# Optimization experiments

Measured on AMD Instinct MI355X. Metric: run time of the kernel, lower is better.

## Reference

```python
import jax, jax.numpy as jnp
import numpy as np

N, L, C, H = 8, 2048, 512, 512
C_HALF = max(C // 2, 1)


def setup_inputs() -> dict:
    key = jax.random.key(0)
    ks = jax.random.split(key, 11)
    s = 0.02
    return {
        "x": jax.random.normal(ks[0], (N, L, C), dtype=jnp.float32),
        "theta_w": jax.random.normal(ks[1], (C, H), dtype=jnp.float32) * s,
        "theta_b": jax.random.normal(ks[2], (H,), dtype=jnp.float32) * s,
        "phi_w": jax.random.normal(ks[3], (C, H), dtype=jnp.float32) * s,
        "phi_b": jax.random.normal(ks[4], (H,), dtype=jnp.float32) * s,
        "psi_w": jax.random.normal(ks[5], (C, H), dtype=jnp.float32) * s,
        "psi_b": jax.random.normal(ks[6], (H,), dtype=jnp.float32) * s,
        "r1_w": jax.random.normal(ks[7], (H, C_HALF), dtype=jnp.float32) * s,
        "r1_b": jax.random.normal(ks[8], (C_HALF,), dtype=jnp.float32) * s,
        "r2_w": jax.random.normal(ks[9], (C_HALF, C), dtype=jnp.float32) * s,
        "r2_b": jax.random.normal(ks[10], (C,), dtype=jnp.float32) * s,
    }


def reference(x, theta_w, theta_b, phi_w, phi_b, psi_w, psi_b, r1_w, r1_b, r2_w, r2_b):
    # projections: [n, L, h]
    x_t = x @ theta_w + theta_b
    x_ph = x @ phi_w + phi_b
    x_psi = x @ psi_w + psi_b
    # unscaled attention: phi @ theta^T -> [n, L, L], softmax over last dim
    attn = jax.nn.softmax(jnp.einsum("nlh,nmh->nlm", x_ph, x_t), axis=2)
    x_add = jnp.einsum("nlm,nmh->nlh", attn, x_psi)
    # recover MLP with LeakyReLU(0.2) then Tanh, residual add
    h1 = jax.nn.leaky_relu(x_add @ r1_w + r1_b, negative_slope=0.2)
    h2 = jnp.tanh(h1 @ r2_w + r2_b)
    return x + h2
```

## Files before the change

kernel.cpp:

```cpp
#include <hip/hip_runtime.h>
#include <hip/hip_bf16.h>

typedef float f32x4 __attribute__((ext_vector_type(4)));
typedef int   v8i   __attribute__((ext_vector_type(8)));
typedef __attribute__((address_space(3))) unsigned int       lds_uint;
typedef __attribute__((address_space(1))) const unsigned int glb_uint;

__device__ __forceinline__ float tanh_fast(float x) {
    float e = __expf(-2.0f * fabsf(x));
    float r = (1.0f - e) / (1.0f + e);
    return copysignf(r, x);
}
__device__ __forceinline__ unsigned char f2fp8(float v) {
    return (unsigned char)(__builtin_amdgcn_cvt_pk_fp8_f32(v, 0.0f, 0, false) & 0xff);
}
__device__ __forceinline__ unsigned short f2h(float v) {
    _Float16 h = (_Float16)v;
    unsigned short u;
    __builtin_memcpy(&u, &h, 2);
    return u;
}
__device__ __forceinline__ float h2f(unsigned short u) {
    _Float16 h;
    __builtin_memcpy(&h, &u, 2);
    return (float)h;
}

__global__ __launch_bounds__(256) void prep(
    const float* __restrict__ x,
    const float* __restrict__ theta_w, const float* __restrict__ phi_w,
    const float* __restrict__ psi_w,   const float* __restrict__ r1_w,
    const float* __restrict__ r2_w,
    const float* __restrict__ theta_b, const float* __restrict__ phi_b,
    const float* __restrict__ psi_b,
    unsigned char* __restrict__ xb8, unsigned char* __restrict__ wCat8T,
    unsigned char* __restrict__ r1T8, unsigned char* __restrict__ r2T8,
    float* __restrict__ bCat) {
    const int b = blockIdx.x, t = threadIdx.x;
    if (b < 8192) {
        long i = ((long)b * 256 + t) * 4;
        float4 f = *(const float4*)(x + i);
        int w = __builtin_amdgcn_cvt_pk_fp8_f32(f.x, f.y, 0, false);
        w = __builtin_amdgcn_cvt_pk_fp8_f32(f.z, f.w, w, true);
        *(unsigned int*)(xb8 + i) = (unsigned int)w;
    } else if (b < 11264) {
        const int sel = (b - 8192) >> 10;
        const int idx = ((b - 8192) & 1023) * 256 + t;
        const float* w = sel == 0 ? theta_w : (sel == 1 ? phi_w : psi_w);
        const int r = idx >> 9, c = idx & 511;
        wCat8T[(long)(sel * 512 + c) * 512 + r] = f2fp8(w[idx] * 16.0f);
    } else if (b < 11776) {
        const int idx = (b - 11264) * 256 + t;
        const int r = idx >> 8, c = idx & 255;
        r1T8[(long)c * 512 + r] = f2fp8(r1_w[idx] * 16.0f);
    } else if (b < 12288) {
        const int idx = (b - 11776) * 256 + t;
        const int r = idx >> 9, c = idx & 511;
        r2T8[(long)c * 256 + r] = f2fp8(r2_w[idx] * 16.0f);
    } else {
        const int i = (b - 12288) * 256 + t;
        if (i < 1536)
            bCat[i] = i < 512 ? theta_b[i] : (i < 1024 ? phi_b[i - 512] : psi_b[i - 1024]);
    }
}

__global__ __launch_bounds__(256) void softmax_fp8(unsigned short* __restrict__ S) {
    const size_t row = (size_t)blockIdx.y * 2048 + blockIdx.x;
    unsigned short* p = S + row * 2048;
    const int t = threadIdx.x;
    uint4 raw = *(uint4*)(p + t * 8);
    unsigned int w[4] = {raw.x, raw.y, raw.z, raw.w};
    float v[8];
#pragma unroll
    for (int i = 0; i < 4; ++i) {
        v[2 * i]     = h2f((unsigned short)(w[i] & 0xffffu));
        v[2 * i + 1] = h2f((unsigned short)(w[i] >> 16));
    }
    float mx = v[0];
#pragma unroll
    for (int i = 1; i < 8; ++i) mx = fmaxf(mx, v[i]);
#pragma unroll
    for (int off = 32; off > 0; off >>= 1) mx = fmaxf(mx, __shfl_xor(mx, off));
    __shared__ float red[8];
    const int wave = t >> 6, lane = t & 63;
    if (lane == 0) red[wave] = mx;
    __syncthreads();
    mx = fmaxf(fmaxf(red[0], red[1]), fmaxf(red[2], red[3]));
    float s = 0.0f;
#pragma unroll
    for (int i = 0; i < 8; ++i) { v[i] = __expf(v[i] - mx); s += v[i]; }
#pragma unroll
    for (int off = 32; off > 0; off >>= 1) s += __shfl_xor(s, off);
    if (lane == 0) red[4 + wave] = s;
    __syncthreads();
    s = red[4] + red[5] + red[6] + red[7];
    const float inv = 1.0f / s;
    int o0 = __builtin_amdgcn_cvt_pk_fp8_f32(v[0] * inv, v[1] * inv, 0, false);
    o0 = __builtin_amdgcn_cvt_pk_fp8_f32(v[2] * inv, v[3] * inv, o0, true);
    int o1 = __builtin_amdgcn_cvt_pk_fp8_f32(v[4] * inv, v[5] * inv, 0, false);
    o1 = __builtin_amdgcn_cvt_pk_fp8_f32(v[6] * inv, v[7] * inv, o1, true);
    uint2 ov; ov.x = (unsigned int)o0; ov.y = (unsigned int)o1;
    *(uint2*)((unsigned char*)p + t * 8) = ov;
}

template <int MODE>
__global__ __launch_bounds__(256) void gemm_fp8(
    const unsigned char* __restrict__ A,
    const unsigned char* __restrict__ Bt,
    const float* __restrict__ bias,
    const float* __restrict__ resid,
    unsigned short* __restrict__ outH,
    unsigned char* __restrict__ out8,
    unsigned char* __restrict__ out8b,
    unsigned char* __restrict__ outV,
    float* __restrict__ outF,
    int K, int ldaB, int ldbB, int ldc, long sA, long sB, long sC) {
    __shared__ unsigned char As[2][128 * 128];
    __shared__ unsigned char Bs[2][128 * 128];

    const int tid  = threadIdx.x;
    const int lane = tid & 63, wave = tid >> 6;
    const int m16  = lane & 15, quad = lane >> 4;
    const int wm   = (wave >> 1) << 6, wn = (wave & 1) << 6;
    const int m0   = blockIdx.x << 7, n0 = blockIdx.y << 7;

    const int srow = lane >> 3;
    const int uswz = (lane & 7) ^ srow;

    const unsigned char* Abase = A  + (long)blockIdx.z * sA + (long)m0 * ldaB;
    const unsigned char* Bbase = Bt + (long)blockIdx.z * sB + (long)n0 * ldbB;
    const int stR = (wave << 5) + srow;
    const long gA0 = (long)stR * ldaB + (uswz << 4);
    const long gB0 = (long)stR * ldbB + (uswz << 4);

    const int s8  = m16 & 7;
    const int P   = quad ^ (s8 >> 1);
    const int cLo = (P << 1) + (s8 & 1);
    const int offLo = cLo << 4;
    const int offHi = (cLo ^ 1) << 4;

    f32x4 acc[4][4] = {};

    union F8 { v8i v; int4 q[2]; };

    auto STAGE = [&](int buf, int kk) {
#pragma unroll
        for (int i = 0; i < 4; ++i) {
            const unsigned char* gp = Abase + gA0 + (long)(i << 3) * ldaB + kk;
            unsigned char* lp = &As[buf][((wave << 5) + (i << 3)) << 7];
            __builtin_amdgcn_global_load_lds((glb_uint*)gp, (lds_uint*)lp, 16, 0, 0);
        }
#pragma unroll
        for (int i = 0; i < 4; ++i) {
            const unsigned char* gp = Bbase + gB0 + (long)(i << 3) * ldbB + kk;
            unsigned char* lp = &Bs[buf][((wave << 5) + (i << 3)) << 7];
            __builtin_amdgcn_global_load_lds((glb_uint*)gp, (lds_uint*)lp, 16, 0, 0);
        }
    };

    STAGE(0, 0);
    int cur = 0;
    for (int k0 = 0; k0 < K; k0 += 128) {
        if (k0 + 128 < K) {
            STAGE(cur ^ 1, k0 + 128);
            asm volatile("s_waitcnt vmcnt(8)" ::: "memory");
        } else {
            asm volatile("s_waitcnt vmcnt(0)" ::: "memory");
        }
        asm volatile("s_barrier" ::: "memory");

        const unsigned char* Ab = As[cur];
        const unsigned char* Bb = Bs[cur];
        F8 af[4], bg[4];
#pragma unroll
        for (int f = 0; f < 4; ++f) {
            const int m = wm + (f << 4) + m16;
            const int n = wn + (f << 4) + m16;
            af[f].q[0] = *(const int4*)&Ab[(m << 7) + offLo];
            af[f].q[1] = *(const int4*)&Ab[(m << 7) + offHi];
            bg[f].q[0] = *(const int4*)&Bb[(n << 7) + offLo];
            bg[f].q[1] = *(const int4*)&Bb[(n << 7) + offHi];
        }
#pragma unroll
        for (int fi = 0; fi < 4; ++fi)
#pragma unroll
            for (int fj = 0; fj < 4; ++fj)
                acc[fi][fj] = __builtin_amdgcn_mfma_scale_f32_16x16x128_f8f6f4(
                    af[fi].v, bg[fj].v, acc[fi][fj],
                    0, 0,
                    0, 127,
                    0, 127);

        asm volatile("s_waitcnt lgkmcnt(0)" ::: "memory");
        asm volatile("s_barrier" ::: "memory");
        cur ^= 1;
    }

    const long zC = (long)blockIdx.z * sC;

    if (MODE == 0) {
        const int sel = n0 >> 9;
        if (sel < 2) {
            unsigned char* dst = sel == 0 ? out8 : out8b;
#pragma unroll
            for (int fj = 0; fj < 4; ++fj) {
                const int col = n0 + wn + (fj << 4) + m16;
                const int cb  = col & 511;
                const float bv = bias[col];
#pragma unroll
                for (int fi = 0; fi < 4; ++fi)
#pragma unroll
                    for (int r = 0; r < 4; ++r) {
                        const int row = m0 + wm + (fi << 4) + (quad << 2) + r;
                        dst[(long)row * 512 + cb] = f2fp8(acc[fi][fj][r] * 0.0625f + bv);
                    }
            }
        } else {
            const int z = m0 >> 11, l0 = (m0 & 2047) + wm + (quad << 2);
#pragma unroll
            for (int fj = 0; fj < 4; ++fj) {
                const int col = n0 + wn + (fj << 4) + m16;
                const int h   = col & 511;
                const float bv = bias[col];
#pragma unroll
                for (int fi = 0; fi < 4; ++fi) {
                    int w = __builtin_amdgcn_cvt_pk_fp8_f32(
                        acc[fi][fj][0] * 0.0625f + bv, acc[fi][fj][1] * 0.0625f + bv, 0, false);
                    w = __builtin_amdgcn_cvt_pk_fp8_f32(
                        acc[fi][fj][2] * 0.0625f + bv, acc[fi][fj][3] * 0.0625f + bv, w, true);
                    *(unsigned int*)(outV + ((long)z * 512 + h) * 2048 + l0 + (fi << 4)) =
                        (unsigned int)w;
                }
            }
        }
    } else {
#pragma unroll
        for (int fj = 0; fj < 4; ++fj) {
            const int col = n0 + wn + (fj << 4) + m16;
            float bv = 0.0f;
            if (MODE >= 3) bv = bias[col];
#pragma unroll
            for (int fi = 0; fi < 4; ++fi)
#pragma unroll
                for (int r = 0; r < 4; ++r) {
                    const int row = m0 + wm + (fi << 4) + (quad << 2) + r;
                    float v = acc[fi][fj][r];
                    if (MODE == 1) {
                        outH[zC + (long)row * ldc + col] = f2h(v);
                    } else if (MODE == 2) {
                        out8[zC + (long)row * 512 + col] = f2fp8(v);
                    } else if (MODE == 3) {
                        v = v * 0.0625f + bv;
                        v = v > 0.0f ? v : 0.2f * v;
                        out8[(long)row * 256 + col] = f2fp8(v);
                    } else {
                        v = v * 0.0625f + bv;
                        const long idx = (long)row * ldc + col;
                        outF[idx] = tanh_fast(v) + resid[idx];
                    }
                }
        }
    }
}

extern "C" void kernel_launch(void* const* d_in, const int* in_sizes, int n_in,
                              void* d_out, int out_size, void* d_ws, size_t ws_size,
                              hipStream_t stream) {
    const float* x       = (const float*)d_in[0];
    const float* theta_w = (const float*)d_in[1];
    const float* theta_b = (const float*)d_in[2];
    const float* phi_w   = (const float*)d_in[3];
    const float* phi_b   = (const float*)d_in[4];
    const float* psi_w   = (const float*)d_in[5];
    const float* psi_b   = (const float*)d_in[6];
    const float* r1_w    = (const float*)d_in[7];
    const float* r1_b    = (const float*)d_in[8];
    const float* r2_w    = (const float*)d_in[9];
    const float* r2_b    = (const float*)d_in[10];
    float* out = (float*)d_out;

    constexpr int  N = 8, L = 2048, C = 512, H = 512, CH = 256;
    constexpr long NL = (long)N * L;

    char* p = (char*)d_ws;
    auto alloc = [&](size_t bytes) { void* q = (void*)p; p += bytes; return q; };
    unsigned char*  xb8    = (unsigned char*)alloc(NL * C);
    unsigned char*  TH8    = (unsigned char*)alloc(NL * H);
    unsigned char*  PH8    = (unsigned char*)alloc(NL * H);
    unsigned char*  VT8    = (unsigned char*)alloc((long)N * H * L);
    unsigned char*  xadd8  = (unsigned char*)alloc(NL * H);
    unsigned char*  h18    = (unsigned char*)alloc(NL * CH);
    unsigned char*  wCat8T = (unsigned char*)alloc((long)1536 * 512);
    unsigned char*  r1T8   = (unsigned char*)alloc((long)H * CH);
    unsigned char*  r2T8   = (unsigned char*)alloc((long)CH * C);
    float*          bCat   = (float*)alloc(1536 * 4 + 256);
    unsigned short* S      = (unsigned short*)alloc((long)N * L * L * 2);

    prep<<<12294, 256, 0, stream>>>(x, theta_w, phi_w, psi_w, r1_w, r2_w,
                                    theta_b, phi_b, psi_b, xb8, wCat8T, r1T8, r2T8, bCat);

    gemm_fp8<0><<<dim3(NL / 128, 1536 / 128, 1), 256, 0, stream>>>(
        xb8, wCat8T, bCat, nullptr, nullptr, TH8, PH8, VT8, nullptr,
        C, C, C, 0, 0, 0, 0);

    gemm_fp8<1><<<dim3(L / 128, L / 128, N), 256, 0, stream>>>(
        PH8, TH8, nullptr, nullptr, S, nullptr, nullptr, nullptr, nullptr,
        H, H, H, L, (long)L * H, (long)L * H, (long)L * L);

    softmax_fp8<<<dim3(L, N), 256, 0, stream>>>(S);

    gemm_fp8<2><<<dim3(L / 128, H / 128, N), 256, 0, stream>>>(
        (const unsigned char*)S, VT8, nullptr, nullptr, nullptr, xadd8, nullptr, nullptr, nullptr,
        L, 2 * L, L, H, (long)L * 2 * L, (long)H * L, (long)L * H);

    gemm_fp8<3><<<dim3(NL / 128, CH / 128, 1), 256, 0, stream>>>(
        xadd8, r1T8, r1_b, nullptr, nullptr, h18, nullptr, nullptr, nullptr,
        H, H, H, CH, 0, 0, 0);

    gemm_fp8<4><<<dim3(NL / 128, C / 128, 1), 256, 0, stream>>>(
        h18, r2T8, r2_b, x, nullptr, nullptr, nullptr, nullptr, out,
        CH, CH, CH, C, 0, 0, 0);
}
```

Baseline: 223.6 us.

## Add 256x256-tile 512-thread GEMM for projection and score stages

Adds a new fp8 GEMM kernel that uses 256x256 output tiles with 8 waves, each computing a 128x64 sub-tile. It is used for the fused QKV projection and for the phi·theta^T score GEMM, and it loads A fragments one at a time inside the loop to limit register pressure. Larger tiles raise data reuse per byte staged in LDS. The cost is 128KB of double-buffered LDS per block, which limits occupancy to one block per CU despite the launch bounds, and the grid has fewer blocks. The smaller GEMMs keep the 128x128 kernel, whose epilogue is trimmed to their modes.

```diff
diff --git a/kernel.cpp b/kernel.cpp
--- a/kernel.cpp
+++ b/kernel.cpp
@@ -109,10 +109,7 @@
     const unsigned char* __restrict__ Bt,
     const float* __restrict__ bias,
     const float* __restrict__ resid,
-    unsigned short* __restrict__ outH,
     unsigned char* __restrict__ out8,
-    unsigned char* __restrict__ out8b,
-    unsigned char* __restrict__ outV,
     float* __restrict__ outF,
     int K, int ldaB, int ldbB, int ldc, long sA, long sB, long sC) {
     __shared__ unsigned char As[2][128 * 128];
@@ -140,7 +137,6 @@
     const int offHi = (cLo ^ 1) << 4;
 
     f32x4 acc[4][4] = {};
-
     union F8 { v8i v; int4 q[2]; };
 
     auto STAGE = [&](int buf, int kk) {
@@ -187,9 +183,126 @@
             for (int fj = 0; fj < 4; ++fj)
                 acc[fi][fj] = __builtin_amdgcn_mfma_scale_f32_16x16x128_f8f6f4(
                     af[fi].v, bg[fj].v, acc[fi][fj],
-                    0, 0,
-                    0, 127,
-                    0, 127);
+                    0, 0, 0, 127, 0, 127);
+
+        asm volatile("s_waitcnt lgkmcnt(0)" ::: "memory");
+        asm volatile("s_barrier" ::: "memory");
+        cur ^= 1;
+    }
+
+    const long zC = (long)blockIdx.z * sC;
+
+#pragma unroll
+    for (int fj = 0; fj < 4; ++fj) {
+        const int col = n0 + wn + (fj << 4) + m16;
+        float bv = 0.0f;
+        if (MODE >= 3) bv = bias[col];
+#pragma unroll
+        for (int fi = 0; fi < 4; ++fi)
+#pragma unroll
+            for (int r = 0; r < 4; ++r) {
+                const int row = m0 + wm + (fi << 4) + (quad << 2) + r;
+                float v = acc[fi][fj][r];
+                if (MODE == 2) {
+                    out8[zC + (long)row * 512 + col] = f2fp8(v);
+                } else if (MODE == 3) {
+                    v = v * 0.0625f + bv;
+                    v = v > 0.0f ? v : 0.2f * v;
+                    out8[(long)row * 256 + col] = f2fp8(v);
+                } else {
+                    v = v * 0.0625f + bv;
+                    const long idx = (long)row * ldc + col;
+                    outF[idx] = tanh_fast(v) + resid[idx];
+                }
+            }
+    }
+}
+
+template <int MODE>
+__global__ __launch_bounds__(512, 2) void gemm_fp8_big(
+    const unsigned char* __restrict__ A,
+    const unsigned char* __restrict__ Bt,
+    const float* __restrict__ bias,
+    unsigned short* __restrict__ outH,
+    unsigned char* __restrict__ out8,
+    unsigned char* __restrict__ out8b,
+    unsigned char* __restrict__ outV,
+    int K, int ldaB, int ldbB, int ldc, long sA, long sB, long sC) {
+    __shared__ unsigned char As[2][256 * 128];
+    __shared__ unsigned char Bs[2][256 * 128];
+
+    const int tid  = threadIdx.x;
+    const int lane = tid & 63, wave = tid >> 6;
+    const int m16  = lane & 15, quad = lane >> 4;
+    const int wm   = (wave >> 2) << 7;
+    const int wn   = (wave & 3) << 6;
+    const int m0   = blockIdx.x << 8, n0 = blockIdx.y << 8;
+
+    const int srow = lane >> 3;
+    const int uswz = (lane & 7) ^ srow;
+
+    const unsigned char* Abase = A  + (long)blockIdx.z * sA + (long)m0 * ldaB;
+    const unsigned char* Bbase = Bt + (long)blockIdx.z * sB + (long)n0 * ldbB;
+    const int stR = (wave << 5) + srow;
+    const long gA0 = (long)stR * ldaB + (uswz << 4);
+    const long gB0 = (long)stR * ldbB + (uswz << 4);
+
+    const int s8  = m16 & 7;
+    const int P   = quad ^ (s8 >> 1);
+    const int cLo = (P << 1) + (s8 & 1);
+    const int offLo = cLo << 4;
+    const int offHi = (cLo ^ 1) << 4;
+
+    f32x4 acc[8][4] = {};
+    union F8 { v8i v; int4 q[2]; };
+
+    auto STAGE = [&](int buf, int kk) {
+#pragma unroll
+        for (int i = 0; i < 4; ++i) {
+            const unsigned char* gp = Abase + gA0 + (long)(i << 3) * ldaB + kk;
+            unsigned char* lp = &As[buf][((wave << 5) + (i << 3)) << 7];
+            __builtin_amdgcn_global_load_lds((glb_uint*)gp, (lds_uint*)lp, 16, 0, 0);
+        }
+#pragma unroll
+        for (int i = 0; i < 4; ++i) {
+            const unsigned char* gp = Bbase + gB0 + (long)(i << 3) * ldbB + kk;
+            unsigned char* lp = &Bs[buf][((wave << 5) + (i << 3)) << 7];
+            __builtin_amdgcn_global_load_lds((glb_uint*)gp, (lds_uint*)lp, 16, 0, 0);
+        }
+    };
+
+    STAGE(0, 0);
+    int cur = 0;
+    for (int k0 = 0; k0 < K; k0 += 128) {
+        if (k0 + 128 < K) {
+            STAGE(cur ^ 1, k0 + 128);
+            asm volatile("s_waitcnt vmcnt(8)" ::: "memory");
+        } else {
+            asm volatile("s_waitcnt vmcnt(0)" ::: "memory");
+        }
+        asm volatile("s_barrier" ::: "memory");
+
+        const unsigned char* Ab = As[cur];
+        const unsigned char* Bb = Bs[cur];
+        F8 bg[4];
+#pragma unroll
+        for (int fj = 0; fj < 4; ++fj) {
+            const int n = wn + (fj << 4) + m16;
+            bg[fj].q[0] = *(const int4*)&Bb[(n << 7) + offLo];
+            bg[fj].q[1] = *(const int4*)&Bb[(n << 7) + offHi];
+        }
+#pragma unroll
+        for (int fi = 0; fi < 8; ++fi) {
+            F8 af;
+            const int m = wm + (fi << 4) + m16;
+            af.q[0] = *(const int4*)&Ab[(m << 7) + offLo];
+            af.q[1] = *(const int4*)&Ab[(m << 7) + offHi];
+#pragma unroll
+            for (int fj = 0; fj < 4; ++fj)
+                acc[fi][fj] = __builtin_amdgcn_mfma_scale_f32_16x16x128_f8f6f4(
+                    af.v, bg[fj].v, acc[fi][fj],
+                    0, 0, 0, 127, 0, 127);
+        }
 
         asm volatile("s_waitcnt lgkmcnt(0)" ::: "memory");
         asm volatile("s_barrier" ::: "memory");
@@ -208,7 +321,7 @@
                 const int cb  = col & 511;
                 const float bv = bias[col];
 #pragma unroll
-                for (int fi = 0; fi < 4; ++fi)
+                for (int fi = 0; fi < 8; ++fi)
 #pragma unroll
                     for (int r = 0; r < 4; ++r) {
                         const int row = m0 + wm + (fi << 4) + (quad << 2) + r;
@@ -223,7 +336,7 @@
                 const int h   = col & 511;
                 const float bv = bias[col];
 #pragma unroll
-                for (int fi = 0; fi < 4; ++fi) {
+                for (int fi = 0; fi < 8; ++fi) {
                     int w = __builtin_amdgcn_cvt_pk_fp8_f32(
                         acc[fi][fj][0] * 0.0625f + bv, acc[fi][fj][1] * 0.0625f + bv, 0, false);
                     w = __builtin_amdgcn_cvt_pk_fp8_f32(
@@ -237,27 +350,12 @@
 #pragma unroll
         for (int fj = 0; fj < 4; ++fj) {
             const int col = n0 + wn + (fj << 4) + m16;
-            float bv = 0.0f;
-            if (MODE >= 3) bv = bias[col];
-#pragma unroll
-            for (int fi = 0; fi < 4; ++fi)
+#pragma unroll
+            for (int fi = 0; fi < 8; ++fi)
 #pragma unroll
                 for (int r = 0; r < 4; ++r) {
                     const int row = m0 + wm + (fi << 4) + (quad << 2) + r;
-                    float v = acc[fi][fj][r];
-                    if (MODE == 1) {
-                        outH[zC + (long)row * ldc + col] = f2h(v);
-                    } else if (MODE == 2) {
-                        out8[zC + (long)row * 512 + col] = f2fp8(v);
-                    } else if (MODE == 3) {
-                        v = v * 0.0625f + bv;
-                        v = v > 0.0f ? v : 0.2f * v;
-                        out8[(long)row * 256 + col] = f2fp8(v);
-                    } else {
-                        v = v * 0.0625f + bv;
-                        const long idx = (long)row * ldc + col;
-                        outF[idx] = tanh_fast(v) + resid[idx];
-                    }
+                    outH[zC + (long)row * ldc + col] = f2h(acc[fi][fj][r]);
                 }
         }
     }
@@ -299,25 +397,25 @@
     prep<<<12294, 256, 0, stream>>>(x, theta_w, phi_w, psi_w, r1_w, r2_w,
                                     theta_b, phi_b, psi_b, xb8, wCat8T, r1T8, r2T8, bCat);
 
-    gemm_fp8<0><<<dim3(NL / 128, 1536 / 128, 1), 256, 0, stream>>>(
-        xb8, wCat8T, bCat, nullptr, nullptr, TH8, PH8, VT8, nullptr,
+    gemm_fp8_big<0><<<dim3(NL / 256, 1536 / 256, 1), 512, 0, stream>>>(
+        xb8, wCat8T, bCat, nullptr, TH8, PH8, VT8,
         C, C, C, 0, 0, 0, 0);
 
-    gemm_fp8<1><<<dim3(L / 128, L / 128, N), 256, 0, stream>>>(
-        PH8, TH8, nullptr, nullptr, S, nullptr, nullptr, nullptr, nullptr,
+    gemm_fp8_big<1><<<dim3(L / 256, L / 256, N), 512, 0, stream>>>(
+        PH8, TH8, nullptr, S, nullptr, nullptr, nullptr,
         H, H, H, L, (long)L * H, (long)L * H, (long)L * L);
 
     softmax_fp8<<<dim3(L, N), 256, 0, stream>>>(S);
 
     gemm_fp8<2><<<dim3(L / 128, H / 128, N), 256, 0, stream>>>(
-        (const unsigned char*)S, VT8, nullptr, nullptr, nullptr, xadd8, nullptr, nullptr, nullptr,
+        (const unsigned char*)S, VT8, nullptr, nullptr, xadd8, nullptr,
         L, 2 * L, L, H, (long)L * 2 * L, (long)H * L, (long)L * H);
 
     gemm_fp8<3><<<dim3(NL / 128, CH / 128, 1), 256, 0, stream>>>(
-        xadd8, r1T8, r1_b, nullptr, nullptr, h18, nullptr, nullptr, nullptr,
+        xadd8, r1T8, r1_b, nullptr, h18, nullptr,
         H, H, H, CH, 0, 0, 0);
 
     gemm_fp8<4><<<dim3(NL / 128, C / 128, 1), 256, 0, stream>>>(
-        h18, r2T8, r2_b, x, nullptr, nullptr, nullptr, nullptr, out,
+        h18, r2T8, r2_b, x, nullptr, out,
         CH, CH, CH, C, 0, 0, 0);
 }
```

Result: no change. 227.9 us (+1.9%).

## Fuse attention score, softmax and PV GEMMs into a flash-attention kernel

Applied to the files above, without the earlier changes.

Replaces the separate QK^T GEMM, the fp16 score write, the softmax pass and the PV GEMM with one flash-style kernel that keeps scores on chip and uses an online softmax with running max and sum. This removes the round trips of the 8x2048x2048 score matrix through global memory and two kernel launches. In exchange the new kernel uses 512-thread blocks with large LDS buffers, only 256 blocks, and many barriers per chunk, so occupancy and sync overhead could limit it. P is rescaled by 256 before fp8 conversion to keep precision.

```diff
diff --git a/kernel.cpp b/kernel.cpp
--- a/kernel.cpp
+++ b/kernel.cpp
@@ -13,17 +13,6 @@
 }
 __device__ __forceinline__ unsigned char f2fp8(float v) {
     return (unsigned char)(__builtin_amdgcn_cvt_pk_fp8_f32(v, 0.0f, 0, false) & 0xff);
-}
-__device__ __forceinline__ unsigned short f2h(float v) {
-    _Float16 h = (_Float16)v;
-    unsigned short u;
-    __builtin_memcpy(&u, &h, 2);
-    return u;
-}
-__device__ __forceinline__ float h2f(unsigned short u) {
-    _Float16 h;
-    __builtin_memcpy(&h, &u, 2);
-    return (float)h;
 }
 
 __global__ __launch_bounds__(256) void prep(
@@ -64,52 +53,12 @@
     }
 }
 
-__global__ __launch_bounds__(256) void softmax_fp8(unsigned short* __restrict__ S) {
-    const size_t row = (size_t)blockIdx.y * 2048 + blockIdx.x;
-    unsigned short* p = S + row * 2048;
-    const int t = threadIdx.x;
-    uint4 raw = *(uint4*)(p + t * 8);
-    unsigned int w[4] = {raw.x, raw.y, raw.z, raw.w};
-    float v[8];
-#pragma unroll
-    for (int i = 0; i < 4; ++i) {
-        v[2 * i]     = h2f((unsigned short)(w[i] & 0xffffu));
-        v[2 * i + 1] = h2f((unsigned short)(w[i] >> 16));
-    }
-    float mx = v[0];
-#pragma unroll
-    for (int i = 1; i < 8; ++i) mx = fmaxf(mx, v[i]);
-#pragma unroll
-    for (int off = 32; off > 0; off >>= 1) mx = fmaxf(mx, __shfl_xor(mx, off));
-    __shared__ float red[8];
-    const int wave = t >> 6, lane = t & 63;
-    if (lane == 0) red[wave] = mx;
-    __syncthreads();
-    mx = fmaxf(fmaxf(red[0], red[1]), fmaxf(red[2], red[3]));
-    float s = 0.0f;
-#pragma unroll
-    for (int i = 0; i < 8; ++i) { v[i] = __expf(v[i] - mx); s += v[i]; }
-#pragma unroll
-    for (int off = 32; off > 0; off >>= 1) s += __shfl_xor(s, off);
-    if (lane == 0) red[4 + wave] = s;
-    __syncthreads();
-    s = red[4] + red[5] + red[6] + red[7];
-    const float inv = 1.0f / s;
-    int o0 = __builtin_amdgcn_cvt_pk_fp8_f32(v[0] * inv, v[1] * inv, 0, false);
-    o0 = __builtin_amdgcn_cvt_pk_fp8_f32(v[2] * inv, v[3] * inv, o0, true);
-    int o1 = __builtin_amdgcn_cvt_pk_fp8_f32(v[4] * inv, v[5] * inv, 0, false);
-    o1 = __builtin_amdgcn_cvt_pk_fp8_f32(v[6] * inv, v[7] * inv, o1, true);
-    uint2 ov; ov.x = (unsigned int)o0; ov.y = (unsigned int)o1;
-    *(uint2*)((unsigned char*)p + t * 8) = ov;
-}
-
 template <int MODE>
 __global__ __launch_bounds__(256) void gemm_fp8(
     const unsigned char* __restrict__ A,
     const unsigned char* __restrict__ Bt,
     const float* __restrict__ bias,
     const float* __restrict__ resid,
-    unsigned short* __restrict__ outH,
     unsigned char* __restrict__ out8,
     unsigned char* __restrict__ out8b,
     unsigned char* __restrict__ outV,
@@ -140,7 +89,6 @@
     const int offHi = (cLo ^ 1) << 4;
 
     f32x4 acc[4][4] = {};
-
     union F8 { v8i v; int4 q[2]; };
 
     auto STAGE = [&](int buf, int kk) {
@@ -187,16 +135,12 @@
             for (int fj = 0; fj < 4; ++fj)
                 acc[fi][fj] = __builtin_amdgcn_mfma_scale_f32_16x16x128_f8f6f4(
                     af[fi].v, bg[fj].v, acc[fi][fj],
-                    0, 0,
-                    0, 127,
-                    0, 127);
+                    0, 0, 0, 127, 0, 127);
 
         asm volatile("s_waitcnt lgkmcnt(0)" ::: "memory");
         asm volatile("s_barrier" ::: "memory");
         cur ^= 1;
     }
-
-    const long zC = (long)blockIdx.z * sC;
 
     if (MODE == 0) {
         const int sel = n0 >> 9;
@@ -237,30 +181,256 @@
 #pragma unroll
         for (int fj = 0; fj < 4; ++fj) {
             const int col = n0 + wn + (fj << 4) + m16;
-            float bv = 0.0f;
-            if (MODE >= 3) bv = bias[col];
+            const float bv = bias[col];
 #pragma unroll
             for (int fi = 0; fi < 4; ++fi)
 #pragma unroll
                 for (int r = 0; r < 4; ++r) {
                     const int row = m0 + wm + (fi << 4) + (quad << 2) + r;
-                    float v = acc[fi][fj][r];
-                    if (MODE == 1) {
-                        outH[zC + (long)row * ldc + col] = f2h(v);
-                    } else if (MODE == 2) {
-                        out8[zC + (long)row * 512 + col] = f2fp8(v);
-                    } else if (MODE == 3) {
-                        v = v * 0.0625f + bv;
+                    float v = acc[fi][fj][r] * 0.0625f + bv;
+                    if (MODE == 3) {
                         v = v > 0.0f ? v : 0.2f * v;
                         out8[(long)row * 256 + col] = f2fp8(v);
                     } else {
-                        v = v * 0.0625f + bv;
                         const long idx = (long)row * ldc + col;
                         outF[idx] = tanh_fast(v) + resid[idx];
                     }
                 }
         }
     }
+}
+
+__global__ __launch_bounds__(512) void flash(
+    const unsigned char* __restrict__ Qg8,
+    const unsigned char* __restrict__ Kg8,
+    const unsigned char* __restrict__ Vg8,
+    unsigned char* __restrict__ out8) {
+    __shared__ unsigned char Qs[64 * 512];
+    __shared__ unsigned char Ks[2][128 * 128];
+    __shared__ unsigned char Vs[512 * 128];
+    __shared__ unsigned char Ps[64 * 128];
+    __shared__ float smax[2][32][4];
+    __shared__ float ssum[2][32][4];
+
+    const int tid  = threadIdx.x;
+    const int lane = tid & 63, wave = tid >> 6;
+    const int m16  = lane & 15, quad = lane >> 4;
+    const int lg   = wave >> 2;
+    const int mw   = wave & 3;
+    const int z    = blockIdx.y;
+    const int l0   = blockIdx.x << 6;
+
+    const unsigned char* Qg = Qg8 + ((long)z * 2048 + l0) * 512;
+    const unsigned char* Kg = Kg8 + (long)z * 2048 * 512;
+    const unsigned char* Vg = Vg8 + (long)z * 512 * 2048;
+
+    const int s8  = m16 & 7;
+    const int cLo = ((quad ^ (s8 >> 1)) << 1) + (s8 & 1);
+    const int offLo = cLo << 4, offHi = (cLo ^ 1) << 4;
+
+    auto stageQ = [&]() {
+#pragma unroll
+        for (int i = 0; i < 4; ++i) {
+            const int slot = wave * 4 + i;
+            const int row  = slot * 2 + (lane >> 5);
+            const int w5   = lane & 31;
+            const int su   = (w5 & 24) | ((w5 & 7) ^ (row & 7));
+            const unsigned char* gp = Qg + (long)row * 512 + (su << 4);
+            __builtin_amdgcn_global_load_lds((glb_uint*)gp, (lds_uint*)&Qs[slot << 10], 16, 0, 0);
+        }
+    };
+    auto stageK = [&](int t) {
+        const int c = t >> 2, ks = t & 3;
+#pragma unroll
+        for (int i = 0; i < 2; ++i) {
+            const int slot = wave * 2 + i;
+            const int row  = (slot << 3) + (lane >> 3);
+            const int su   = (lane & 7) ^ (row & 7);
+            const unsigned char* gp = Kg + (long)(c * 128 + row) * 512 + ks * 128 + (su << 4);
+            __builtin_amdgcn_global_load_lds((glb_uint*)gp, (lds_uint*)&Ks[t & 1][slot << 10], 16, 0, 0);
+        }
+    };
+    auto stageV = [&](int c) {
+#pragma unroll
+        for (int i = 0; i < 8; ++i) {
+            const int slot = wave * 8 + i;
+            const int row  = (slot << 3) + (lane >> 3);
+            const int su   = (lane & 7) ^ (row & 7);
+            const unsigned char* gp = Vg + (long)row * 2048 + c * 128 + (su << 4);
+            __builtin_amdgcn_global_load_lds((glb_uint*)gp, (lds_uint*)&Vs[slot << 10], 16, 0, 0);
+        }
+    };
+
+    f32x4 U[2][8] = {};
+    float m_run[2][4], l_run[2][4];
+#pragma unroll
+    for (int a = 0; a < 2; ++a)
+#pragma unroll
+        for (int b = 0; b < 4; ++b) { m_run[a][b] = -3.0e38f; l_run[a][b] = 0.0f; }
+
+    union F8 { v8i v; int4 q[2]; };
+
+    stageQ();
+    stageK(0);
+
+    for (int c = 0; c < 16; ++c) {
+        f32x4 sacc[2][2] = {};
+#pragma unroll
+        for (int ks = 0; ks < 4; ++ks) {
+            const int t = c * 4 + ks;
+            if (t + 1 < 64) stageK(t + 1);
+            if (ks == 1) stageV(c);
+            if (ks == 0) {
+                asm volatile("s_waitcnt vmcnt(2)" ::: "memory");
+            } else if (ks == 3) {
+                if (c == 15) asm volatile("s_waitcnt vmcnt(0)" ::: "memory");
+                else         asm volatile("s_waitcnt vmcnt(2)" ::: "memory");
+            } else {
+                asm volatile("s_waitcnt vmcnt(10)" ::: "memory");
+            }
+            asm volatile("s_barrier" ::: "memory");
+
+            const unsigned char* Kb = Ks[t & 1];
+            F8 aq[2], bk[2];
+#pragma unroll
+            for (int f = 0; f < 2; ++f) {
+                const int l = lg * 32 + f * 16 + m16;
+                aq[f].q[0] = *(const int4*)&Qs[l * 512 + ks * 128 + offLo];
+                aq[f].q[1] = *(const int4*)&Qs[l * 512 + ks * 128 + offHi];
+                const int m = mw * 32 + f * 16 + m16;
+                bk[f].q[0] = *(const int4*)&Kb[(m << 7) + offLo];
+                bk[f].q[1] = *(const int4*)&Kb[(m << 7) + offHi];
+            }
+#pragma unroll
+            for (int fi = 0; fi < 2; ++fi)
+#pragma unroll
+                for (int fj = 0; fj < 2; ++fj)
+                    sacc[fi][fj] = __builtin_amdgcn_mfma_scale_f32_16x16x128_f8f6f4(
+                        aq[fi].v, bk[fj].v, sacc[fi][fj], 0, 0, 0, 127, 0, 127);
+
+            asm volatile("s_waitcnt lgkmcnt(0)" ::: "memory");
+            asm volatile("s_barrier" ::: "memory");
+        }
+
+        float pm[2][4];
+#pragma unroll
+        for (int fi = 0; fi < 2; ++fi)
+#pragma unroll
+            for (int r = 0; r < 4; ++r) {
+                float v = fmaxf(sacc[fi][0][r], sacc[fi][1][r]);
+#pragma unroll
+                for (int off = 1; off < 16; off <<= 1) v = fmaxf(v, __shfl_xor(v, off));
+                pm[fi][r] = v;
+            }
+        if (m16 == 0) {
+#pragma unroll
+            for (int fi = 0; fi < 2; ++fi)
+#pragma unroll
+                for (int r = 0; r < 4; ++r)
+                    smax[lg][fi * 16 + quad * 4 + r][mw] = pm[fi][r];
+        }
+        asm volatile("s_waitcnt lgkmcnt(0)" ::: "memory");
+        asm volatile("s_barrier" ::: "memory");
+
+        float alpha[2][4], p[2][2][4];
+#pragma unroll
+        for (int fi = 0; fi < 2; ++fi)
+#pragma unroll
+            for (int r = 0; r < 4; ++r) {
+                const int rr = fi * 16 + quad * 4 + r;
+                float cm = fmaxf(fmaxf(smax[lg][rr][0], smax[lg][rr][1]),
+                                 fmaxf(smax[lg][rr][2], smax[lg][rr][3]));
+                const float mo = m_run[fi][r];
+                const float mn = fmaxf(mo, cm);
+                m_run[fi][r] = mn;
+                alpha[fi][r] = __expf(mo - mn);
+#pragma unroll
+                for (int fj = 0; fj < 2; ++fj)
+                    p[fi][fj][r] = __expf(sacc[fi][fj][r] - mn);
+            }
+#pragma unroll
+        for (int fi = 0; fi < 2; ++fi)
+#pragma unroll
+            for (int fh = 0; fh < 8; ++fh)
+#pragma unroll
+                for (int r = 0; r < 4; ++r)
+                    U[fi][fh][r] *= alpha[fi][r];
+        float ps[2][4];
+#pragma unroll
+        for (int fi = 0; fi < 2; ++fi)
+#pragma unroll
+            for (int r = 0; r < 4; ++r) {
+                float v = p[fi][0][r] + p[fi][1][r];
+#pragma unroll
+                for (int off = 1; off < 16; off <<= 1) v += __shfl_xor(v, off);
+                ps[fi][r] = v;
+            }
+        if (m16 == 0) {
+#pragma unroll
+            for (int fi = 0; fi < 2; ++fi)
+#pragma unroll
+                for (int r = 0; r < 4; ++r)
+                    ssum[lg][fi * 16 + quad * 4 + r][mw] = ps[fi][r];
+        }
+#pragma unroll
+        for (int fi = 0; fi < 2; ++fi)
+#pragma unroll
+            for (int r = 0; r < 4; ++r) {
+                const int l = lg * 32 + fi * 16 + quad * 4 + r;
+#pragma unroll
+                for (int fj = 0; fj < 2; ++fj) {
+                    const int m = mw * 32 + fj * 16 + m16;
+                    Ps[(l << 7) + ((((m >> 4) ^ (l & 7)) << 4) | (m & 15))] =
+                        f2fp8(p[fi][fj][r] * 256.0f);
+                }
+            }
+        asm volatile("s_waitcnt vmcnt(2) lgkmcnt(0)" ::: "memory");
+        asm volatile("s_barrier" ::: "memory");
+
+#pragma unroll
+        for (int fi = 0; fi < 2; ++fi)
+#pragma unroll
+            for (int r = 0; r < 4; ++r) {
+                const int rr = fi * 16 + quad * 4 + r;
+                l_run[fi][r] = l_run[fi][r] * alpha[fi][r] +
+                               ssum[lg][rr][0] + ssum[lg][rr][1] +
+                               ssum[lg][rr][2] + ssum[lg][rr][3];
+            }
+
+        F8 pa[2];
+#pragma unroll
+        for (int f = 0; f < 2; ++f) {
+            const int l = lg * 32 + f * 16 + m16;
+            pa[f].q[0] = *(const int4*)&Ps[(l << 7) + offLo];
+            pa[f].q[1] = *(const int4*)&Ps[(l << 7) + offHi];
+        }
+#pragma unroll
+        for (int fh = 0; fh < 8; ++fh) {
+            F8 vb;
+            const int h = mw * 128 + fh * 16 + m16;
+            vb.q[0] = *(const int4*)&Vs[(h << 7) + offLo];
+            vb.q[1] = *(const int4*)&Vs[(h << 7) + offHi];
+#pragma unroll
+            for (int fi = 0; fi < 2; ++fi)
+                U[fi][fh] = __builtin_amdgcn_mfma_scale_f32_16x16x128_f8f6f4(
+                    pa[fi].v, vb.v, U[fi][fh], 0, 0, 0, 127, 0, 127);
+        }
+        asm volatile("s_waitcnt lgkmcnt(0)" ::: "memory");
+        asm volatile("s_barrier" ::: "memory");
+    }
+
+#pragma unroll
+    for (int fi = 0; fi < 2; ++fi)
+#pragma unroll
+        for (int r = 0; r < 4; ++r) {
+            const float inv = 1.0f / (256.0f * l_run[fi][r]);
+            const long row = (long)z * 2048 + l0 + lg * 32 + fi * 16 + quad * 4 + r;
+#pragma unroll
+            for (int fh = 0; fh < 8; ++fh) {
+                const int h = mw * 128 + fh * 16 + m16;
+                out8[row * 512 + h] = f2fp8(U[fi][fh][r] * inv);
+            }
+        }
 }
 
 extern "C" void kernel_launch(void* const* d_in, const int* in_sizes, int n_in,
@@ -294,30 +464,21 @@
     unsigned char*  r1T8   = (unsigned char*)alloc((long)H * CH);
     unsigned char*  r2T8   = (unsigned char*)alloc((long)CH * C);
     float*          bCat   = (float*)alloc(1536 * 4 + 256);
-    unsigned short* S      = (unsigned short*)alloc((long)N * L * L * 2);
 
     prep<<<12294, 256, 0, stream>>>(x, theta_w, phi_w, psi_w, r1_w, r2_w,
                                     theta_b, phi_b, psi_b, xb8, wCat8T, r1T8, r2T8, bCat);
 
     gemm_fp8<0><<<dim3(NL / 128, 1536 / 128, 1), 256, 0, stream>>>(
-        xb8, wCat8T, bCat, nullptr, nullptr, TH8, PH8, VT8, nullptr,
+        xb8, wCat8T, bCat, nullptr, TH8, PH8, VT8, nullptr,
         C, C, C, 0, 0, 0, 0);
 
-    gemm_fp8<1><<<dim3(L / 128, L / 128, N), 256, 0, stream>>>(
-        PH8, TH8, nullptr, nullptr, S, nullptr, nullptr, nullptr, nullptr,
-        H, H, H, L, (long)L * H, (long)L * H, (long)L * L);
-
-    softmax_fp8<<<dim3(L, N), 256, 0, stream>>>(S);
-
-    gemm_fp8<2><<<dim3(L / 128, H / 128, N), 256, 0, stream>>>(
-        (const unsigned char*)S, VT8, nullptr, nullptr, nullptr, xadd8, nullptr, nullptr, nullptr,
-        L, 2 * L, L, H, (long)L * 2 * L, (long)H * L, (long)L * H);
+    flash<<<dim3(L / 64, N, 1), 512, 0, stream>>>(PH8, TH8, VT8, xadd8);
 
     gemm_fp8<3><<<dim3(NL / 128, CH / 128, 1), 256, 0, stream>>>(
-        xadd8, r1T8, r1_b, nullptr, nullptr, h18, nullptr, nullptr, nullptr,
+        xadd8, r1T8, r1_b, nullptr, h18, nullptr, nullptr, nullptr,
         H, H, H, CH, 0, 0, 0);
 
     gemm_fp8<4><<<dim3(NL / 128, C / 128, 1), 256, 0, stream>>>(
-        h18, r2T8, r2_b, x, nullptr, nullptr, nullptr, nullptr, out,
+        h18, r2T8, r2_b, x, nullptr, nullptr, nullptr, out,
         CH, CH, CH, C, 0, 0, 0);
 }
```

After: 257.9 us. 1.15x slower.
